# Performance work log

Measured on AMD Instinct MI355X. Metric: run time of the kernel, lower is better.

The kernel has to match this reference:

```python
import jax, jax.numpy as jnp
import numpy as np

N = 100000       # nodes
E = 1600000      # edges (avg degree 16)
D_IN = 128
D_HID = 32
D_OUT = 32
H = 4            # heads
NEG_SLOPE = 0.2  # GATConv default leaky_relu slope


def setup_inputs() -> dict:
    key = jax.random.key(0)
    ks = jax.random.split(key, 10)
    s = 0.1
    return {
        "edge": jax.random.randint(ks[0], (2, E), 0, N),
        "features": jax.random.normal(ks[1], (N, D_IN), jnp.float32),
        # layer 1 params: W [in, H*hid], attention vectors per head [H, hid]
        "W1": jax.random.normal(ks[2], (D_IN, H * D_HID), jnp.float32) * s,
        "a1_src": jax.random.normal(ks[3], (H, D_HID), jnp.float32) * s,
        "a1_dst": jax.random.normal(ks[4], (H, D_HID), jnp.float32) * s,
        "b1": jnp.zeros((H * D_HID,), jnp.float32),
        # layer 2 params
        "W2": jax.random.normal(ks[5], (H * D_HID, H * D_OUT), jnp.float32) * s,
        "a2_src": jax.random.normal(ks[6], (H, D_OUT), jnp.float32) * s,
        "a2_dst": jax.random.normal(ks[7], (H, D_OUT), jnp.float32) * s,
        "b2": jnp.zeros((H * D_OUT,), jnp.float32),
    }


def gat_conv(x, src, dst, W, a_src, a_dst, b, heads, d_out):
    """Multi-head GAT layer, concat heads. x: [N, d_in] -> [N, heads*d_out]."""
    n = x.shape[0]
    h = (x @ W).reshape(n, heads, d_out)                 # [N,H,D]
    e_src = jnp.einsum('nhd,hd->nh', h, a_src)           # [N,H]
    e_dst = jnp.einsum('nhd,hd->nh', h, a_dst)           # [N,H]
    e = jax.nn.leaky_relu(e_src[src] + e_dst[dst], NEG_SLOPE)  # [E,H]
    # softmax over incoming edges of each dst node (stable via segment max)
    m = jax.lax.stop_gradient(jax.ops.segment_max(e, dst, num_segments=n))
    w = jnp.exp(e - m[dst])                              # [E,H]
    den = jax.ops.segment_sum(w, dst, num_segments=n)    # [N,H]
    alpha = w / den[dst]                                 # [E,H]
    out = jax.ops.segment_sum(alpha[:, :, None] * h[src], dst, num_segments=n)
    return out.reshape(n, heads * d_out) + b


def reference(edge, features, W1, a1_src, a1_dst, b1, W2, a2_src, a2_dst, b2):
    src, dst = edge[0], edge[1]
    h = jax.nn.relu(gat_conv(features, src, dst, W1, a1_src, a1_dst, b1, H, D_HID))
    h = gat_conv(h, src, dst, W2, a2_src, a2_dst, b2, H, D_OUT)
    return jax.nn.log_softmax(h, axis=1)
```

## Files before the change

kernel.cpp:

```cpp
#include <hip/hip_runtime.h>
#include <hip/hip_bf16.h>
#include <math.h>

#define N_NODES 100000
#define N_EDGES 1600000
#define NHEADS 4
#define NEG_SLOPE 0.2f
#define NSUP 196
#define SSHIFT 9
#define SMASK 511
#define CHUNK 4096
#define NBLK ((N_EDGES + CHUNK - 1) / CHUNK)
#define LCAP 72
#define SCAP 9216
#define CPAD 16

typedef __attribute__((ext_vector_type(8))) short short8;
typedef __attribute__((ext_vector_type(4))) float f32x4;
typedef __attribute__((ext_vector_type(2))) float f32x2;

__device__ __forceinline__ unsigned short f2bf(float f) {
    unsigned int u = __float_as_uint(f);
    u += 0x7fffu + ((u >> 16) & 1u);
    return (unsigned short)(u >> 16);
}
__device__ __forceinline__ f32x2 bfpair(unsigned int u) {
    f32x2 r;
    r.x = __uint_as_float(u << 16);
    r.y = __uint_as_float(u & 0xffff0000u);
    return r;
}
__device__ __forceinline__ short8 pack8(float4 f0, float4 f1) {
    short8 v;
    v[0] = (short)f2bf(f0.x); v[1] = (short)f2bf(f0.y);
    v[2] = (short)f2bf(f0.z); v[3] = (short)f2bf(f0.w);
    v[4] = (short)f2bf(f1.x); v[5] = (short)f2bf(f1.y);
    v[6] = (short)f2bf(f1.z); v[7] = (short)f2bf(f1.w);
    return v;
}

__global__ void pack_w_kernel(const float* __restrict__ W1,
                              const float* __restrict__ a1s,
                              const float* __restrict__ a1d,
                              const float* __restrict__ W2,
                              const float* __restrict__ a2s,
                              const float* __restrict__ a2d,
                              unsigned short* __restrict__ Wp1,
                              unsigned short* __restrict__ Wp2,
                              int* __restrict__ cursors) {
    if (blockIdx.x >= 144) {
        for (int i = threadIdx.x; i < NSUP * CPAD; i += 256) cursors[i] = 0;
        return;
    }
    const int which = blockIdx.x >= 72;
    const float* W      = which ? W2 : W1;
    const float* a_src  = which ? a2s : a1s;
    const float* a_dst  = which ? a2d : a1d;
    unsigned short* Wp  = which ? Wp2 : Wp1;
    int idx = (blockIdx.x - (which ? 72 : 0)) * 256 + threadIdx.x;
    int j    = idx & 7;
    int lane = (idx >> 3) & 63;
    int kc   = (idx >> 9) & 3;
    int ct   = idx >> 11;
    int k = kc * 32 + ((lane >> 4) & 3) * 8 + j;
    int n = lane & 15;
    float v = 0.f;
    if (ct < 8) {
        v = W[k * 128 + ct * 16 + n];
    } else if (n < 8) {
        int hd = n & 3;
        const float* av = (n < 4 ? a_src : a_dst) + hd * 32;
        const float* wr = W + k * 128 + hd * 32;
#pragma unroll
        for (int t = 0; t < 32; ++t) v = fmaf(wr[t], av[t], v);
    }
    Wp[idx] = f2bf(v);
}

template <bool XF32>
__global__ __launch_bounds__(256) void gemm_mfma_kernel(
        const void* __restrict__ xv,
        const unsigned short* __restrict__ Wp,
        unsigned short* __restrict__ h, float* __restrict__ esd, int n_rows) {
    __shared__ unsigned short Wl[18432];

    const int t = threadIdx.x;
    {
        const uint4* s4 = (const uint4*)Wp;
        uint4* d4 = (uint4*)Wl;
#pragma unroll
        for (int p = 0; p < 9; ++p) d4[p * 256 + t] = s4[p * 256 + t];
    }
    __syncthreads();

    const int lane = t & 63, wave = t >> 6;
    const int l15 = lane & 15, quad = lane >> 4;
    const int rbase = blockIdx.x * 128 + wave * 32;

    short8 a[2][4];
#pragma unroll
    for (int rt = 0; rt < 2; ++rt) {
        int r = rbase + rt * 16 + l15;
        r = r < n_rows ? r : n_rows - 1;
        if (XF32) {
            const float* xr = (const float*)xv + (size_t)r * 128 + quad * 8;
#pragma unroll
            for (int kc = 0; kc < 4; ++kc) {
                float4 f0 = *(const float4*)(xr + kc * 32);
                float4 f1 = *(const float4*)(xr + kc * 32 + 4);
                a[rt][kc] = pack8(f0, f1);
            }
        } else {
            const unsigned short* xr =
                (const unsigned short*)xv + (size_t)r * 128 + quad * 8;
#pragma unroll
            for (int kc = 0; kc < 4; ++kc)
                a[rt][kc] = *(const short8*)(xr + kc * 32);
        }
    }

    f32x4 acc[2][9];
#pragma unroll
    for (int rt = 0; rt < 2; ++rt)
#pragma unroll
        for (int ct = 0; ct < 9; ++ct)
            acc[rt][ct] = (f32x4){0.f, 0.f, 0.f, 0.f};

#pragma unroll
    for (int ct = 0; ct < 9; ++ct) {
#pragma unroll
        for (int kc = 0; kc < 4; ++kc) {
            short8 b = *(const short8*)&Wl[((ct * 4 + kc) * 64 + lane) * 8];
            acc[0][ct] = __builtin_amdgcn_mfma_f32_16x16x32_bf16(
                a[0][kc], b, acc[0][ct], 0, 0, 0);
            acc[1][ct] = __builtin_amdgcn_mfma_f32_16x16x32_bf16(
                a[1][kc], b, acc[1][ct], 0, 0, 0);
        }
    }

#pragma unroll
    for (int rt = 0; rt < 2; ++rt) {
#pragma unroll
        for (int i = 0; i < 4; ++i) {
            int r = rbase + rt * 16 + quad * 4 + i;
            if (r < n_rows) {
                unsigned short* hp = h + (size_t)r * 128 + l15;
#pragma unroll
                for (int ct = 0; ct < 8; ++ct)
                    hp[ct * 16] = f2bf(acc[rt][ct][i]);
                if (l15 < 8) esd[r * 8 + l15] = acc[rt][8][i];
            }
        }
    }
}

__global__ __launch_bounds__(256) void scatter_kernel(
        const int* __restrict__ src, const int* __restrict__ dst,
        int* __restrict__ cursors, unsigned int* __restrict__ sslab) {
    __shared__ unsigned int lists[NSUP * LCAP];
    __shared__ int lcnt[NSUP];
    __shared__ int posb[NSUP];
    const int t = threadIdx.x;
    for (int i = t; i < NSUP; i += 256) lcnt[i] = 0;
    __syncthreads();
    const int e0 = blockIdx.x * CHUNK;
#pragma unroll
    for (int k = 0; k < 4; ++k) {
        int e4 = e0 + (k * 256 + t) * 4;
        if (e4 + 3 < N_EDGES) {
            int4 d4 = *(const int4*)(dst + e4);
            int4 s4 = *(const int4*)(src + e4);
            int dd[4] = {d4.x, d4.y, d4.z, d4.w};
            int ss[4] = {s4.x, s4.y, s4.z, s4.w};
#pragma unroll
            for (int j = 0; j < 4; ++j) {
                int su = dd[j] >> SSHIFT;
                int pos = atomicAdd(&lcnt[su], 1);
                if (pos < LCAP)
                    lists[su * LCAP + pos] =
                        (unsigned)ss[j] | ((unsigned)(dd[j] & SMASK) << 17);
            }
        } else {
            for (int j = 0; j < 4; ++j) {
                int e = e4 + j;
                if (e < N_EDGES) {
                    int d = dst[e];
                    int su = d >> SSHIFT;
                    int pos = atomicAdd(&lcnt[su], 1);
                    if (pos < LCAP)
                        lists[su * LCAP + pos] =
                            (unsigned)src[e] | ((unsigned)(d & SMASK) << 17);
                }
            }
        }
    }
    __syncthreads();
    if (t < NSUP) {
        int n = lcnt[t]; n = n > LCAP ? LCAP : n;
        int p = atomicAdd(&cursors[t * CPAD], n);
        int room = SCAP - p; if (room < 0) room = 0;
        if (n > room) n = room;
        posb[t] = p; lcnt[t] = n;
    }
    __syncthreads();
    const int lane = t & 63, wave = t >> 6;
    for (int s = wave; s < NSUP; s += 4) {
        int n = lcnt[s];
        unsigned int* dstp = sslab + (size_t)s * SCAP + posb[s];
        for (int i = lane; i < n; i += 64) dstp[i] = lists[s * LCAP + i];
    }
}

__global__ __launch_bounds__(512) void super_build_kernel(
        const unsigned int* __restrict__ sslab, const int* __restrict__ cursors,
        int* __restrict__ rowptr, int* __restrict__ csr_src) {
    __shared__ int hist[512];
    __shared__ int ws[8];
    __shared__ int lo_sh;
    const int s = blockIdx.x;
    const int t = threadIdx.x, lane = t & 63, wave = t >> 6;

    {
        int val = 0, v = 0;
        if (t < 256) {
            val = (t < NSUP) ? cursors[t * CPAD] : 0;
            v = val;
#pragma unroll
            for (int off = 1; off < 64; off <<= 1) {
                int u = __shfl_up(v, off);
                if (lane >= off) v += u;
            }
            if (lane == 63) ws[wave] = v;
        }
        __syncthreads();
        if (t < 256) {
            int woff = 0, tot = 0;
#pragma unroll
            for (int w = 0; w < 4; ++w) { if (w < wave) woff += ws[w]; tot += ws[w]; }
            if (t == s) lo_sh = woff + v - val;
            if (s == 0 && t == 0) rowptr[N_NODES] = tot;
        }
        __syncthreads();
    }
    const int lo = lo_sh;

    int cnt = cursors[s * CPAD]; if (cnt > SCAP) cnt = SCAP;
    const unsigned int* sp = sslab + (size_t)s * SCAP;
    hist[t] = 0;
    __syncthreads();
    for (int i = t; i < cnt; i += 512)
        atomicAdd(&hist[sp[i] >> 17], 1);
    __syncthreads();
    int val = hist[t];
    int v = val;
#pragma unroll
    for (int off = 1; off < 64; off <<= 1) {
        int u = __shfl_up(v, off);
        if (lane >= off) v += u;
    }
    if (lane == 63) ws[wave] = v;
    __syncthreads();
    int woff = 0;
#pragma unroll
    for (int w = 0; w < 8; ++w) if (w < wave) woff += ws[w];
    int excl = woff + v - val;
    hist[t] = lo + excl;
    int node = s * 512 + t;
    if (node < N_NODES) rowptr[node] = lo + excl;
    __syncthreads();
    for (int i = t; i < cnt; i += 512) {
        unsigned int rec = sp[i];
        int loc = rec >> 17;
        int pos = atomicAdd(&hist[loc], 1);
        csr_src[pos] = (int)(rec & 0x1FFFFu);
    }
}

template <bool LOGSOFTMAX>
__global__ __launch_bounds__(1024) void aggregate_kernel(
        const int* __restrict__ csr_src, const int* __restrict__ rowptr,
        const float* __restrict__ esd,
        const unsigned short* __restrict__ hb, const float* __restrict__ b,
        void* __restrict__ out) {
    const int lane = threadIdx.x & 63;
    const int wave = threadIdx.x >> 6;
    const int n = blockIdx.x * 16 + wave;
    const int eo = lane >> 4;
    const int cl = lane & 15;
    const int c0 = cl * 8;
    const int hd = cl >> 2;
    const float edn = esd[n * 8 + 4 + hd];
    const int base = rowptr[n];
    const int dg = rowptr[n + 1] - base;

    f32x2 acc2[4];
#pragma unroll
    for (int j = 0; j < 4; ++j) acc2[j] = (f32x2){0.f, 0.f};
    float wsum = 0.f;

    if (dg > 0) {
        const int myidx = csr_src[base + (lane < dg ? lane : dg - 1)];
        const int nit = (dg + 3) >> 2;
        const unsigned hbo = (unsigned)c0 * 2u;
        const unsigned edo = (unsigned)hd * 4u;
        const char* hbp = (const char*)hb;
        const char* esp = (const char*)esd;

        auto getS = [&](int j) -> int {
            int o = 4 * j + eo;
            if (4 * j < 64) return __shfl(myidx, o);
            int oc = o < dg ? o : dg - 1;
            return csr_src[base + oc];
        };
        auto loadP = [&](int s) -> uint4 {
            return *(const uint4*)(hbp + (((unsigned)s << 8) + hbo));
        };
        auto loadE = [&](int s, int j) -> float {
            float e = *(const float*)(esp + (((unsigned)s << 5) + edo));
            return (4 * j + eo < dg) ? e : -1e30f;
        };

        int s0 = getS(0);
        uint4 p0 = loadP(s0);
        float e0 = loadE(s0, 0);
        uint4 p1 = p0; float e1 = e0;
        if (nit > 1) {
            int s1 = getS(1);
            p1 = loadP(s1);
            e1 = loadE(s1, 1);
        }
#pragma unroll 2
        for (int j = 0; j < nit; ++j) {
            uint4 p2 = p1; float e2 = e1;
            if (j + 2 < nit) {
                int s2 = getS(j + 2);
                p2 = loadP(s2);
                e2 = loadE(s2, j + 2);
            }
            float sc = e0 + edn;
            sc = sc > 0.f ? sc : NEG_SLOPE * sc;
            float w = __expf(sc);
            f32x2 wv = {w, w};
            acc2[0] = __builtin_elementwise_fma(wv, bfpair(p0.x), acc2[0]);
            acc2[1] = __builtin_elementwise_fma(wv, bfpair(p0.y), acc2[1]);
            acc2[2] = __builtin_elementwise_fma(wv, bfpair(p0.z), acc2[2]);
            acc2[3] = __builtin_elementwise_fma(wv, bfpair(p0.w), acc2[3]);
            wsum += w;
            p0 = p1; e0 = e1; p1 = p2; e1 = e2;
        }
    }

    float acc[8];
#pragma unroll
    for (int j = 0; j < 4; ++j) {
        acc[2 * j]     = acc2[j].x;
        acc[2 * j + 1] = acc2[j].y;
    }

#pragma unroll
    for (int j = 0; j < 8; ++j) {
        acc[j] += __shfl_xor(acc[j], 16);
        acc[j] += __shfl_xor(acc[j], 32);
    }
    wsum += __shfl_xor(wsum, 16);
    wsum += __shfl_xor(wsum, 32);

    float inv = wsum > 0.f ? 1.f / wsum : 0.f;
    float bl[8];
    *(float4*)&bl[0] = *(const float4*)(b + c0);
    *(float4*)&bl[4] = *(const float4*)(b + c0 + 4);
    float v[8];
#pragma unroll
    for (int j = 0; j < 8; ++j) v[j] = acc[j] * inv + bl[j];

    if (!LOGSOFTMAX) {
        if (lane < 16) {
            unsigned int pk[4];
#pragma unroll
            for (int j = 0; j < 4; ++j) {
                float r0 = v[2 * j]     > 0.f ? v[2 * j]     : 0.f;
                float r1 = v[2 * j + 1] > 0.f ? v[2 * j + 1] : 0.f;
                pk[j] = (unsigned int)f2bf(r0) | ((unsigned int)f2bf(r1) << 16);
            }
            *(uint4*)((unsigned short*)out + (size_t)n * 128 + c0) =
                make_uint4(pk[0], pk[1], pk[2], pk[3]);
        }
    } else {
        float m = v[0];
#pragma unroll
        for (int j = 1; j < 8; ++j) m = fmaxf(m, v[j]);
#pragma unroll
        for (int s = 1; s < 16; s <<= 1) m = fmaxf(m, __shfl_xor(m, s));
        float se = 0.f;
#pragma unroll
        for (int j = 0; j < 8; ++j) se += __expf(v[j] - m);
#pragma unroll
        for (int s = 1; s < 16; s <<= 1) se += __shfl_xor(se, s);
        float ls = m + logf(se);
        if (lane < 16) {
            float* o = (float*)out + (size_t)n * 128 + c0;
            *(float4*)o = make_float4(v[0] - ls, v[1] - ls, v[2] - ls, v[3] - ls);
            *(float4*)(o + 4) = make_float4(v[4] - ls, v[5] - ls, v[6] - ls, v[7] - ls);
        }
    }
}

extern "C" void kernel_launch(void* const* d_in, const int* in_sizes, int n_in,
                              void* d_out, int out_size, void* d_ws, size_t ws_size,
                              hipStream_t stream) {
    const int*   edge = (const int*)d_in[0];
    const int*   src  = edge;
    const int*   dst  = edge + N_EDGES;
    const float* feat = (const float*)d_in[1];
    const float* W1   = (const float*)d_in[2];
    const float* a1s  = (const float*)d_in[3];
    const float* a1d  = (const float*)d_in[4];
    const float* b1   = (const float*)d_in[5];
    const float* W2   = (const float*)d_in[6];
    const float* a2s  = (const float*)d_in[7];
    const float* a2d  = (const float*)d_in[8];
    const float* b2   = (const float*)d_in[9];
    float* out = (float*)d_out;

    unsigned short* hb  = (unsigned short*)d_ws;
    unsigned short* x1b = hb + (size_t)N_NODES * 128;
    unsigned short* Wp1 = x1b + (size_t)N_NODES * 128;
    unsigned short* Wp2 = Wp1 + 18432;
    float* esd = (float*)(Wp2 + 18432);
    int* rowptr   = (int*)(esd + (size_t)N_NODES * 8);
    int* cursors  = rowptr + (N_NODES + 1);
    unsigned int* sslab = (unsigned int*)(cursors + NSUP * CPAD);
    int* csr_src  = (int*)(sslab + (size_t)NSUP * SCAP);

    const int gemm_blk  = (N_NODES + 127) / 128;
    const int agg_blk   = N_NODES / 16;

    pack_w_kernel<<<145, 256, 0, stream>>>(W1, a1s, a1d, W2, a2s, a2d,
                                           Wp1, Wp2, cursors);

    scatter_kernel<<<NBLK, 256, 0, stream>>>(src, dst, cursors, sslab);
    super_build_kernel<<<NSUP, 512, 0, stream>>>(sslab, cursors, rowptr, csr_src);

    gemm_mfma_kernel<true><<<gemm_blk, 256, 0, stream>>>(feat, Wp1, hb, esd, N_NODES);
    aggregate_kernel<false><<<agg_blk, 1024, 0, stream>>>(
        csr_src, rowptr, esd, hb, b1, x1b);

    gemm_mfma_kernel<false><<<gemm_blk, 256, 0, stream>>>(x1b, Wp2, hb, esd, N_NODES);
    aggregate_kernel<true><<<agg_blk, 1024, 0, stream>>>(
        csr_src, rowptr, esd, hb, b2, out);
}
```

Measured before the change: 339.1 us.

## Shard scatter cursors into per-block banks and shrink aggregate blocks

Each super-bucket's atomic cursor and slab region is split into 8 banks chosen by block index. This spreads the global atomic contention across banks, and the build kernel now reads all banks and sums their counts. Separately, aggregate kernels launch with 256-thread blocks (4 nodes each) instead of 1024, with a bounds guard, which may improve scheduling granularity. Per-bank capacity of 1200 could overflow and silently drop edges if any bank gets skewed counts.

```diff
diff --git a/kernel.cpp b/kernel.cpp
--- a/kernel.cpp
+++ b/kernel.cpp
@@ -12,7 +12,9 @@
 #define CHUNK 4096
 #define NBLK ((N_EDGES + CHUNK - 1) / CHUNK)
 #define LCAP 72
-#define SCAP 9216
+#define NBANK 8
+#define BCAP2 1200
+#define SCAP (NBANK * BCAP2)
 #define CPAD 16
 
 typedef __attribute__((ext_vector_type(8))) short short8;
@@ -49,7 +51,8 @@
                               unsigned short* __restrict__ Wp2,
                               int* __restrict__ cursors) {
     if (blockIdx.x >= 144) {
-        for (int i = threadIdx.x; i < NSUP * CPAD; i += 256) cursors[i] = 0;
+        for (int i = threadIdx.x; i < NSUP * NBANK * CPAD; i += 256)
+            cursors[i] = 0;
         return;
     }
     const int which = blockIdx.x >= 72;
@@ -163,6 +166,7 @@
     const int t = threadIdx.x;
     for (int i = t; i < NSUP; i += 256) lcnt[i] = 0;
     __syncthreads();
+    const int bank = blockIdx.x & (NBANK - 1);
     const int e0 = blockIdx.x * CHUNK;
 #pragma unroll
     for (int k = 0; k < 4; ++k) {
@@ -197,8 +201,8 @@
     __syncthreads();
     if (t < NSUP) {
         int n = lcnt[t]; n = n > LCAP ? LCAP : n;
-        int p = atomicAdd(&cursors[t * CPAD], n);
-        int room = SCAP - p; if (room < 0) room = 0;
+        int p = atomicAdd(&cursors[(t * NBANK + bank) * CPAD], n);
+        int room = BCAP2 - p; if (room < 0) room = 0;
         if (n > room) n = room;
         posb[t] = p; lcnt[t] = n;
     }
@@ -206,7 +210,7 @@
     const int lane = t & 63, wave = t >> 6;
     for (int s = wave; s < NSUP; s += 4) {
         int n = lcnt[s];
-        unsigned int* dstp = sslab + (size_t)s * SCAP + posb[s];
+        unsigned int* dstp = sslab + (size_t)s * SCAP + bank * BCAP2 + posb[s];
         for (int i = lane; i < n; i += 64) dstp[i] = lists[s * LCAP + i];
     }
 }
@@ -223,7 +227,13 @@
     {
         int val = 0, v = 0;
         if (t < 256) {
-            val = (t < NSUP) ? cursors[t * CPAD] : 0;
+            if (t < NSUP) {
+#pragma unroll
+                for (int k = 0; k < NBANK; ++k) {
+                    int c = cursors[(t * NBANK + k) * CPAD];
+                    val += c > BCAP2 ? BCAP2 : c;
+                }
+            }
             v = val;
 #pragma unroll
             for (int off = 1; off < 64; off <<= 1) {
@@ -244,12 +254,19 @@
     }
     const int lo = lo_sh;
 
-    int cnt = cursors[s * CPAD]; if (cnt > SCAP) cnt = SCAP;
+    int cnt[NBANK];
+#pragma unroll
+    for (int k = 0; k < NBANK; ++k) {
+        int c = cursors[(s * NBANK + k) * CPAD];
+        cnt[k] = c > BCAP2 ? BCAP2 : c;
+    }
     const unsigned int* sp = sslab + (size_t)s * SCAP;
     hist[t] = 0;
     __syncthreads();
-    for (int i = t; i < cnt; i += 512)
-        atomicAdd(&hist[sp[i] >> 17], 1);
+#pragma unroll
+    for (int k = 0; k < NBANK; ++k)
+        for (int i = t; i < cnt[k]; i += 512)
+            atomicAdd(&hist[sp[k * BCAP2 + i] >> 17], 1);
     __syncthreads();
     int val = hist[t];
     int v = val;
@@ -268,23 +285,26 @@
     int node = s * 512 + t;
     if (node < N_NODES) rowptr[node] = lo + excl;
     __syncthreads();
-    for (int i = t; i < cnt; i += 512) {
-        unsigned int rec = sp[i];
-        int loc = rec >> 17;
-        int pos = atomicAdd(&hist[loc], 1);
-        csr_src[pos] = (int)(rec & 0x1FFFFu);
-    }
+#pragma unroll
+    for (int k = 0; k < NBANK; ++k)
+        for (int i = t; i < cnt[k]; i += 512) {
+            unsigned int rec = sp[k * BCAP2 + i];
+            int loc = rec >> 17;
+            int pos = atomicAdd(&hist[loc], 1);
+            csr_src[pos] = (int)(rec & 0x1FFFFu);
+        }
 }
 
 template <bool LOGSOFTMAX>
-__global__ __launch_bounds__(1024) void aggregate_kernel(
+__global__ __launch_bounds__(256) void aggregate_kernel(
         const int* __restrict__ csr_src, const int* __restrict__ rowptr,
         const float* __restrict__ esd,
         const unsigned short* __restrict__ hb, const float* __restrict__ b,
         void* __restrict__ out) {
     const int lane = threadIdx.x & 63;
     const int wave = threadIdx.x >> 6;
-    const int n = blockIdx.x * 16 + wave;
+    const int n = blockIdx.x * 4 + wave;
+    if (n >= N_NODES) return;
     const int eo = lane >> 4;
     const int cl = lane & 15;
     const int c0 = cl * 8;
@@ -429,11 +449,11 @@
     float* esd = (float*)(Wp2 + 18432);
     int* rowptr   = (int*)(esd + (size_t)N_NODES * 8);
     int* cursors  = rowptr + (N_NODES + 1);
-    unsigned int* sslab = (unsigned int*)(cursors + NSUP * CPAD);
+    unsigned int* sslab = (unsigned int*)(cursors + NSUP * NBANK * CPAD);
     int* csr_src  = (int*)(sslab + (size_t)NSUP * SCAP);
 
     const int gemm_blk  = (N_NODES + 127) / 128;
-    const int agg_blk   = N_NODES / 16;
+    const int agg_blk   = (N_NODES + 3) / 4;
 
     pack_w_kernel<<<145, 256, 0, stream>>>(W1, a1s, a1d, W2, a2s, a2d,
                                            Wp1, Wp2, cursors);
@@ -442,10 +462,10 @@
     super_build_kernel<<<NSUP, 512, 0, stream>>>(sslab, cursors, rowptr, csr_src);
 
     gemm_mfma_kernel<true><<<gemm_blk, 256, 0, stream>>>(feat, Wp1, hb, esd, N_NODES);
-    aggregate_kernel<false><<<agg_blk, 1024, 0, stream>>>(
+    aggregate_kernel<false><<<agg_blk, 256, 0, stream>>>(
         csr_src, rowptr, esd, hb, b1, x1b);
 
     gemm_mfma_kernel<false><<<gemm_blk, 256, 0, stream>>>(x1b, Wp2, hb, esd, N_NODES);
-    aggregate_kernel<true><<<agg_blk, 1024, 0, stream>>>(
+    aggregate_kernel<true><<<agg_blk, 256, 0, stream>>>(
         csr_src, rowptr, esd, hb, b2, out);
 }
```

Measured after the change: 330.8 us. 1.02x faster.
